# Performance work log

Hardware: AMD Instinct MI355X
Metric: run time of the kernel (lower is better)

## Reference

```python
import jax, jax.numpy as jnp
import numpy as np

B, L, D, W = 4, 512, 768, 12
K = L * W  # number of candidate spans


def _mlp(x, w1, b1, w2, b2):
    # Linear -> ReLU -> (Dropout=identity in eval) -> Linear
    return jax.nn.relu(x @ w1.T + b1) @ w2.T + b2


def setup_inputs() -> dict:
    key = jax.random.key(0)
    ks = jax.random.split(key, 16)
    sc_d = 1.0 / np.sqrt(D)
    sc_4d = 1.0 / np.sqrt(4 * D)
    sc_2d = 1.0 / np.sqrt(2 * D)
    inp = {
        "h": jax.random.normal(ks[0], (B, L, D), dtype=jnp.float32),
        "span_idx": jax.random.randint(ks[1], (B, K, 2), 0, L, dtype=jnp.int64),
        # project_start: Linear(D,4D), Linear(4D,D)
        "ws1": jax.random.uniform(ks[2], (4 * D, D), jnp.float32, -sc_d, sc_d),
        "bs1": jax.random.uniform(ks[3], (4 * D,), jnp.float32, -sc_d, sc_d),
        "ws2": jax.random.uniform(ks[4], (D, 4 * D), jnp.float32, -sc_4d, sc_4d),
        "bs2": jax.random.uniform(ks[5], (D,), jnp.float32, -sc_4d, sc_4d),
        # project_end
        "we1": jax.random.uniform(ks[6], (4 * D, D), jnp.float32, -sc_d, sc_d),
        "be1": jax.random.uniform(ks[7], (4 * D,), jnp.float32, -sc_d, sc_d),
        "we2": jax.random.uniform(ks[8], (D, 4 * D), jnp.float32, -sc_4d, sc_4d),
        "be2": jax.random.uniform(ks[9], (D,), jnp.float32, -sc_4d, sc_4d),
        # out_project: Linear(2D,4D), Linear(4D,D)
        "wo1": jax.random.uniform(ks[10], (4 * D, 2 * D), jnp.float32, -sc_2d, sc_2d),
        "bo1": jax.random.uniform(ks[11], (4 * D,), jnp.float32, -sc_2d, sc_2d),
        "wo2": jax.random.uniform(ks[12], (D, 4 * D), jnp.float32, -sc_4d, sc_4d),
        "bo2": jax.random.uniform(ks[13], (D,), jnp.float32, -sc_4d, sc_4d),
    }
    return inp


def reference(h, span_idx, ws1, bs1, ws2, bs2, we1, be1, we2, be2, wo1, bo1, wo2, bo2):
    start_rep = _mlp(h, ws1, bs1, ws2, bs2)  # [B, L, D]
    end_rep = _mlp(h, we1, be1, we2, be2)    # [B, L, D]
    bidx = jnp.arange(B)[:, None]
    start_span = start_rep[bidx, span_idx[:, :, 0]]  # gather along seq dim -> [B, K, D]
    end_span = end_rep[bidx, span_idx[:, :, 1]]      # [B, K, D]
    cat = jax.nn.relu(jnp.concatenate([start_span, end_span], axis=-1))  # [B, K, 2D]
    out = _mlp(cat, wo1, bo1, wo2, bo2)  # [B, K, D]
    return out.reshape(B, L, W, D)
```

## Files before the change

kernel.cpp:

```cpp
#include <hip/hip_runtime.h>
#include <hip/hip_bf16.h>

using bf16 = __hip_bfloat16;
using bf16x8 = __attribute__((ext_vector_type(8))) __bf16;
using f32x4  = __attribute__((ext_vector_type(4))) float;
using u32x4  = __attribute__((ext_vector_type(4))) unsigned;
typedef unsigned short ushort_t;

#define BM 128
#define BN 128
#define BK 32


__device__ __forceinline__ void gl_lds16(const void* g, void* l) {
  __builtin_amdgcn_global_load_lds(
      (const __attribute__((address_space(1))) void*)g,
      (__attribute__((address_space(3))) void*)l, 16, 0, 0);
}

__device__ __forceinline__ ushort_t f2bf(float f) {
  unsigned u = __float_as_uint(f);
  u += 0x7FFF + ((u >> 16) & 1);
  return (ushort_t)(u >> 16);
}

__global__ void sniff(const unsigned* __restrict__ w1,
                      const unsigned* __restrict__ idx, int* flags) {
  __shared__ int cnt[2];
  if (threadIdx.x == 0) { cnt[0] = 0; cnt[1] = 0; }
  __syncthreads();
  int t = threadIdx.x;
  int c0 = 0;
  for (int k = 0; k < 4; ++k) {
    unsigned lo = w1[t * 4 + k] & 0xFFFFu;
    unsigned e = (lo >> 7) & 0xFF;
    if (e <= 122) c0++;
  }
  int c1 = (idx[2 * t + 1] != 0) ? 1 : 0;
  atomicAdd(&cnt[0], c0);
  atomicAdd(&cnt[1], c1);
  __syncthreads();
  if (threadIdx.x == 0) {
    flags[0] = (cnt[0] >= 900) ? 1 : 0;
    flags[1] = (cnt[1] == 0) ? 1 : 0;
  }
}

__global__ void norm_idx(const int* __restrict__ flags, const void* __restrict__ src,
                         int* __restrict__ dst) {
  int i = blockIdx.x * 256 + threadIdx.x;
  int v = flags[1] ? (int)((const long long*)src)[i] : ((const int*)src)[i];
  dst[i] = v;
}

__global__ void cvt_all(const int* __restrict__ flags,
                        const void* s0, const void* s1, const void* s2,
                        const void* s3, const void* s4, const void* s5,
                        const void* s6, ushort_t* __restrict__ dst) {
  long i = ((long)blockIdx.x * 256 + threadIdx.x) * 4;
  const void* src; long off;
  if      (i <  1572864) { src = s0; off = i; }
  else if (i <  3932160) { src = s1; off = i - 1572864; }
  else if (i <  6291456) { src = s2; off = i - 3932160; }
  else if (i <  8650752) { src = s3; off = i - 6291456; }
  else if (i < 11010048) { src = s4; off = i - 8650752; }
  else if (i < 15728640) { src = s5; off = i - 11010048; }
  else                   { src = s6; off = i - 15728640; }
  if (flags[0]) {
    *(ushort4*)(dst + i) = *((const ushort4*)((const ushort_t*)src + off));
  } else {
    float4 f = ((const float4*)src)[off >> 2];
    ushort4 o;
    o.x = f2bf(f.x); o.y = f2bf(f.y); o.z = f2bf(f.z); o.w = f2bf(f.w);
    *(ushort4*)(dst + i) = o;
  }
}

__global__ void cvt_bias(const int* __restrict__ flags,
                         const void* b0, const void* b1, const void* b2,
                         const void* b3, const void* b4, const void* b5,
                         float* __restrict__ dst) {
  int i = blockIdx.x * 256 + threadIdx.x;
  if (i >= 14592) return;
  if (i >= 11520) { dst[i] = 0.f; return; }
  const void* src; int off;
  if (i < 3072)       { src = b0; off = i; }
  else if (i < 3840)  { src = b1; off = i - 3072; }
  else if (i < 6912)  { src = b2; off = i - 3840; }
  else if (i < 7680)  { src = b3; off = i - 6912; }
  else if (i < 10752) { src = b4; off = i - 7680; }
  else                { src = b5; off = i - 10752; }
  dst[i] = flags[0] ? __bfloat162float(((const bf16*)src)[off])
                    : ((const float*)src)[off];
}

template <bool GATHER, bool RELU, bool OUTF32>
__global__ __launch_bounds__(256) void gemm_bt(
    const bf16* __restrict__ A, const bf16* __restrict__ A2,
    const bf16* __restrict__ repS, const bf16* __restrict__ repE,
    const int* __restrict__ sidx, int row_base,
    const bf16* __restrict__ Bw, const bf16* __restrict__ Bw2,
    const float* __restrict__ bias, const float* __restrict__ bias2,
    void* __restrict__ C, void* __restrict__ C2, int nsplit,
    int N, int Kdim, int bstride) {
  __shared__ bf16 lA[BM * BK];
  __shared__ bf16 lB[BN * BK];

  const int tid  = threadIdx.x;
  const int lane = tid & 63;
  const int wave = tid >> 6;
  const int wm = wave >> 1, wn = wave & 1;
  int by = blockIdx.y;
  const bf16* Bw_ = Bw; const float* bias_ = bias; void* C_ = C; const bf16* A_ = A;
  if (by >= nsplit) { by -= nsplit; Bw_ = Bw2; bias_ = bias2; C_ = C2; A_ = A2; }
  const int m0 = blockIdx.x * BM;
  const int n0 = by * BN;

  const int srow = tid >> 2;
  const int scol = 8 * ((tid & 3) ^ ((tid >> 3) & 3));

  const bf16 *a0 = nullptr, *a1 = nullptr;
  const bf16 *pS0 = nullptr, *pE0 = nullptr, *pS1 = nullptr, *pE1 = nullptr;
  if (GATHER) {
    int r0 = row_base + m0 + srow;
    int r1 = r0 + 64;
    int b0 = r0 / 6144, b1 = r1 / 6144;
    int s0 = min(max(sidx[2 * r0], 0), 511);
    int e0 = min(max(sidx[2 * r0 + 1], 0), 511);
    int s1 = min(max(sidx[2 * r1], 0), 511);
    int e1 = min(max(sidx[2 * r1 + 1], 0), 511);
    pS0 = repS + ((size_t)b0 * 512 + s0) * 768 + scol;
    pE0 = repE + ((size_t)b0 * 512 + e0) * 768 + scol;
    pS1 = repS + ((size_t)b1 * 512 + s1) * 768 + scol;
    pE1 = repE + ((size_t)b1 * 512 + e1) * 768 + scol;
  } else {
    a0 = A_ + (size_t)(m0 + srow) * Kdim + scol;
    a1 = a0 + (size_t)64 * Kdim;
  }
  const bf16* b0p = Bw_ + (size_t)(n0 + srow) * bstride + scol;
  const bf16* b1p = b0p + (size_t)64 * bstride;

  f32x4 acc[4][4];
  const f32x4 z = {0.f, 0.f, 0.f, 0.f};
#pragma unroll
  for (int i = 0; i < 4; ++i)
#pragma unroll
    for (int j = 0; j < 4; ++j) acc[i][j] = z;

  const int fr = lane & 15;
  const int fk = 8 * ((lane >> 4) ^ ((lane >> 1) & 3));

  for (int k0 = 0; k0 < Kdim; k0 += BK) {
    const bf16 *sa0, *sa1;
    if (GATHER) {
      if (k0 < 768) { sa0 = pS0 + k0; sa1 = pS1 + k0; }
      else          { sa0 = pE0 + (k0 - 768); sa1 = pE1 + (k0 - 768); }
    } else {
      sa0 = a0 + k0; sa1 = a1 + k0;
    }
    gl_lds16(sa0, lA + tid * 8);
    gl_lds16(sa1, lA + 2048 + tid * 8);
    gl_lds16(b0p + k0, lB + tid * 8);
    gl_lds16(b1p + k0, lB + 2048 + tid * 8);
    __syncthreads();

    bf16x8 af[4], bv[4];
#pragma unroll
    for (int i = 0; i < 4; ++i)
      af[i] = *(const bf16x8*)(const void*)(lA + (wm * 64 + i * 16 + fr) * BK + fk);
#pragma unroll
    for (int j = 0; j < 4; ++j)
      bv[j] = *(const bf16x8*)(const void*)(lB + (wn * 64 + j * 16 + fr) * BK + fk);
#pragma unroll
    for (int i = 0; i < 4; ++i)
#pragma unroll
      for (int j = 0; j < 4; ++j)
        acc[i][j] = __builtin_amdgcn_mfma_f32_16x16x32_bf16(af[i], bv[j], acc[i][j], 0, 0, 0);
    __syncthreads();
  }

  float* Cf = (float*)C_;
  bf16*  Cb = (bf16*)C_;
#pragma unroll
  for (int j = 0; j < 4; ++j) {
    int n = n0 + wn * 64 + j * 16 + fr;
    float bj = bias_[n];
#pragma unroll
    for (int i = 0; i < 4; ++i) {
      int mb = m0 + wm * 64 + i * 16 + (lane >> 4) * 4;
#pragma unroll
      for (int r = 0; r < 4; ++r) {
        float v = acc[i][j][r] + bj;
        if (RELU) v = fmaxf(v, 0.f);
        if (OUTF32) Cf[(size_t)(mb + r) * N + n] = v;
        else        Cb[(size_t)(mb + r) * N + n] = __float2bfloat16(v);
      }
    }
  }
}

__global__ __launch_bounds__(256) void gemm_bt64(
    const bf16* __restrict__ A, const bf16* __restrict__ A2,
    const bf16* __restrict__ Bw, const bf16* __restrict__ Bw2,
    const float* __restrict__ bias, const float* __restrict__ bias2,
    bf16* __restrict__ C, bf16* __restrict__ C2, int nsplit,
    int N, int Kdim) {
  __shared__ bf16 lA[64 * BK];
  __shared__ bf16 lB[64 * BK];

  const int tid  = threadIdx.x;
  const int lane = tid & 63;
  const int wave = tid >> 6;
  const int wm = wave >> 1, wn = wave & 1;
  int by = blockIdx.y;
  const bf16* Bw_ = Bw; const float* bias_ = bias; bf16* C_ = C; const bf16* A_ = A;
  if (by >= nsplit) { by -= nsplit; Bw_ = Bw2; bias_ = bias2; C_ = C2; A_ = A2; }
  const int m0 = blockIdx.x * 64;
  const int n0 = by * 64;

  const int srow = tid >> 2;
  const int scol = 8 * ((tid & 3) ^ ((tid >> 3) & 3));

  const bf16* ap = A_  + (size_t)(m0 + srow) * Kdim + scol;
  const bf16* bp = Bw_ + (size_t)(n0 + srow) * Kdim + scol;

  f32x4 acc[2][2];
  const f32x4 z = {0.f, 0.f, 0.f, 0.f};
#pragma unroll
  for (int i = 0; i < 2; ++i)
#pragma unroll
    for (int j = 0; j < 2; ++j) acc[i][j] = z;

  const int fr = lane & 15;
  const int fk = 8 * ((lane >> 4) ^ ((lane >> 1) & 3));

  for (int k0 = 0; k0 < Kdim; k0 += BK) {
    gl_lds16(ap + k0, lA + tid * 8);
    gl_lds16(bp + k0, lB + tid * 8);
    __syncthreads();

    bf16x8 af[2], bv[2];
#pragma unroll
    for (int i = 0; i < 2; ++i)
      af[i] = *(const bf16x8*)(const void*)(lA + (wm * 32 + i * 16 + fr) * BK + fk);
#pragma unroll
    for (int j = 0; j < 2; ++j)
      bv[j] = *(const bf16x8*)(const void*)(lB + (wn * 32 + j * 16 + fr) * BK + fk);
#pragma unroll
    for (int i = 0; i < 2; ++i)
#pragma unroll
      for (int j = 0; j < 2; ++j)
        acc[i][j] = __builtin_amdgcn_mfma_f32_16x16x32_bf16(af[i], bv[j], acc[i][j], 0, 0, 0);
    __syncthreads();
  }

#pragma unroll
  for (int j = 0; j < 2; ++j) {
    int n = n0 + wn * 32 + j * 16 + fr;
    float bj = bias_[n];
#pragma unroll
    for (int i = 0; i < 2; ++i) {
      int mb = m0 + wm * 32 + i * 16 + (lane >> 4) * 4;
#pragma unroll
      for (int r = 0; r < 4; ++r) {
        float v = fmaxf(acc[i][j][r] + bj, 0.f);
        C_[(size_t)(mb + r) * N + n] = __float2bfloat16(v);
      }
    }
  }
}

__global__ __launch_bounds__(512) void gemm_final_fused(
    const ushort_t* __restrict__ Ps, const ushort_t* __restrict__ Pe,
    const int* __restrict__ sidx,
    const bf16* __restrict__ Bw, const float* __restrict__ bias,
    float* __restrict__ out) {
  __shared__ bf16 lA[2 * 4096];
  __shared__ bf16 lB[2 * 16384];

  const int tid  = threadIdx.x;
  const int lane = tid & 63;
  const int wave = tid >> 6;
  const int wm = wave >> 2, wn = wave & 3;
  const int m0 = blockIdx.x * 64;
  const int n0 = blockIdx.y * 256;

  const int t8   = tid & 255;
  const int ksub = tid >> 8;
  const int srow = t8 >> 2;
  const int scol = 8 * ((t8 & 3) ^ ((t8 >> 3) & 3));

  int r0 = m0 + srow;
  int b0 = r0 / 6144;
  int s0 = min(max(sidx[2 * r0], 0), 511);
  int e0 = min(max(sidx[2 * r0 + 1], 0), 511);
  const ushort_t* pS0 = Ps + ((size_t)b0 * 512 + s0) * 3072 + ksub * 32 + scol;
  const ushort_t* pE0 = Pe + ((size_t)b0 * 512 + e0) * 3072 + ksub * 32 + scol;
  const int aoff = ksub * 2048 + t8 * 8;

  const bf16* bp = Bw + (size_t)(n0 + srow) * 3072 + ksub * 32 + scol;
  const int boff = ksub * 8192 + t8 * 8;

  f32x4 acc[2][4];
  const f32x4 z = {0.f, 0.f, 0.f, 0.f};
#pragma unroll
  for (int i = 0; i < 2; ++i)
#pragma unroll
    for (int j = 0; j < 4; ++j) acc[i][j] = z;

  const int fr = lane & 15;
  const int fk = 8 * ((lane >> 4) ^ ((lane >> 1) & 3));

  auto pack_store = [&](u32x4 xs, u32x4 xe, bf16* dst) {
    u32x4 wv;
#pragma unroll
    for (int q = 0; q < 4; ++q) {
      float lo = fmaxf(__uint_as_float(xs[q] << 16) + __uint_as_float(xe[q] << 16), 0.f);
      float hi = fmaxf(__uint_as_float(xs[q] & 0xFFFF0000u) +
                       __uint_as_float(xe[q] & 0xFFFF0000u), 0.f);
      unsigned w;
      asm("v_cvt_pk_bf16_f32 %0, %1, %2" : "=v"(w) : "v"(lo), "v"(hi));
      wv[q] = w;
    }
    *(u32x4*)(void*)dst = wv;
  };

  auto stageB = [&](int k0, int buf) {
#pragma unroll
    for (int g = 0; g < 4; ++g)
      gl_lds16(bp + (size_t)g * 64 * 3072 + k0, lB + buf + boff + g * 2048);
  };

  {
    u32x4 xs = *(const u32x4*)(const void*)pS0;
    u32x4 xe = *(const u32x4*)(const void*)pE0;
    stageB(0, 0);
    pack_store(xs, xe, lA + aoff);
    __syncthreads();
  }

  for (int it = 0; it < 48; ++it) {
    const int curA = (it & 1) << 12;
    const int curB = (it & 1) << 14;
    const int nxtA = curA ^ 4096;
    const int nxtB = curB ^ 16384;
    const int k1 = (it + 1) * 64;
    const bool pre = (it + 1) < 48;
    u32x4 xs, xe;
    if (pre) {
      xs = *(const u32x4*)(const void*)(pS0 + k1);
      xe = *(const u32x4*)(const void*)(pE0 + k1);
      stageB(k1, nxtB);
    }

#pragma unroll
    for (int s = 0; s < 2; ++s) {
      bf16x8 af[2];
#pragma unroll
      for (int i = 0; i < 2; ++i)
        af[i] = *(const bf16x8*)(const void*)(
            lA + curA + s * 2048 + (wm * 32 + i * 16 + fr) * 32 + fk);
#pragma unroll
      for (int j = 0; j < 4; ++j) {
        bf16x8 bv = *(const bf16x8*)(const void*)(
            lB + curB + s * 8192 + (wn * 64 + j * 16 + fr) * 32 + fk);
#pragma unroll
        for (int i = 0; i < 2; ++i)
          acc[i][j] = __builtin_amdgcn_mfma_f32_16x16x32_bf16(af[i], bv, acc[i][j], 0, 0, 0);
      }
    }

    if (pre) {
      pack_store(xs, xe, lA + nxtA + aoff);
    }
    __syncthreads();
  }

#pragma unroll
  for (int j = 0; j < 4; ++j) {
    int n = n0 + wn * 64 + j * 16 + fr;
    float bj = bias[n];
#pragma unroll
    for (int i = 0; i < 2; ++i) {
      int mb = m0 + wm * 32 + i * 16 + (lane >> 4) * 4;
#pragma unroll
      for (int r = 0; r < 4; ++r)
        out[(size_t)(mb + r) * 768 + n] = acc[i][j][r] + bj;
    }
  }
}

extern "C" void kernel_launch(void* const* d_in, const int* in_sizes, int n_in,
                              void* d_out, int out_size, void* d_ws, size_t ws_size,
                              hipStream_t stream) {
  const void* h    = d_in[0];
  const void* sidx = d_in[1];
  const void *ws1 = d_in[2],  *bs1 = d_in[3];
  const void *ws2 = d_in[4],  *bs2 = d_in[5];
  const void *we1 = d_in[6],  *be1 = d_in[7];
  const void *we2 = d_in[8],  *be2 = d_in[9];
  const void *wo1 = d_in[10], *bo1 = d_in[11];
  const void *wo2 = d_in[12], *bo2 = d_in[13];

  char* p = (char*)d_ws;
  int*      flags = (int*)p;
  int*      idx32 = (int*)(p + 256);
  float*    biasf = (float*)(p + 256 + 196608);
  ushort_t* hb    = (ushort_t*)(p + 256 + 196608 + 65536);
  ushort_t* w1sb  = hb   + (size_t)1572864;
  ushort_t* w2sb  = w1sb + (size_t)2359296;
  ushort_t* w1eb  = w2sb + (size_t)2359296;
  ushort_t* w2eb  = w1eb + (size_t)2359296;
  ushort_t* wo1b  = w2eb + (size_t)2359296;
  ushort_t* wo2b  = wo1b + (size_t)4718592;
  ushort_t* repS  = wo2b + (size_t)2359296;
  ushort_t* repE  = repS + (size_t)1572864;
  char*     R     = (char*)(repE + (size_t)1572864);
  size_t fixed = (size_t)(R - (char*)d_ws);
  if (ws_size < fixed) return;
  size_t Rsz = ws_size - fixed;

  const size_t P_BF = (size_t)2 * 2048 * 3072 * 2;
  int tier = (Rsz >= P_BF) ? 2 : 3;

  dim3 blk(256);
  const int XBIG = 0x40000000;
  sniff<<<1, blk, 0, stream>>>((const unsigned*)ws1, (const unsigned*)sidx, flags);
  norm_idx<<<192, blk, 0, stream>>>(flags, sidx, idx32);
  cvt_all<<<17664, blk, 0, stream>>>(flags, h, ws1, ws2, we1, we2, wo1, wo2, hb);
  cvt_bias<<<57, blk, 0, stream>>>(flags, bs1, bs2, be1, be2, bo1, bo2, biasf);
  const float *bs1f = biasf, *bs2f = biasf + 3072, *be1f = biasf + 3840,
              *be2f = biasf + 6912, *bo1f = biasf + 7680, *bo2f = biasf + 10752,
              *zerof = biasf + 11520;
  float* outf = (float*)d_out;

  if (tier == 2) {
    ushort_t* hidS = (ushort_t*)R;
    ushort_t* hidE = hidS + (size_t)2048 * 3072;
    gemm_bt<false, true, false><<<dim3(16, 48), blk, 0, stream>>>(
        (const bf16*)hb, (const bf16*)hb, nullptr, nullptr, nullptr, 0,
        (const bf16*)w1sb, (const bf16*)w1eb, bs1f, be1f,
        hidS, hidE, 24, 3072, 768, 768);
    gemm_bt64<<<dim3(32, 24), blk, 0, stream>>>(
        (const bf16*)hidS, (const bf16*)hidE,
        (const bf16*)w2sb, (const bf16*)w2eb, bs2f, be2f,
        (bf16*)repS, (bf16*)repE, 12, 768, 3072);
    ushort_t* Ps = (ushort_t*)R;
    ushort_t* Pe = Ps + (size_t)2048 * 3072;
    gemm_bt<false, false, false><<<dim3(16, 48), blk, 0, stream>>>(
        (const bf16*)repS, (const bf16*)repE, nullptr, nullptr, nullptr, 0,
        (const bf16*)wo1b, (const bf16*)wo1b + 768, bo1f, zerof,
        Ps, Pe, 24, 3072, 768, 1536);
    gemm_final_fused<<<dim3(384, 3), dim3(512), 0, stream>>>(
        Ps, Pe, idx32, (const bf16*)wo2b, bo2f, outf);
  } else {
    long long cT = (long long)(Rsz / ((size_t)2 * 3072 * 2));
    cT = (cT / 128) * 128; if (cT > 2048) cT = 2048;
    long long cO = (long long)(Rsz / ((size_t)3072 * 2));
    cO = (cO / 128) * 128; if (cO > 24576) cO = 24576;
    if (cT < 128 || cO < 128) return;
    ushort_t* scr = (ushort_t*)R;
    for (long long r = 0; r < 2048; r += cT) {
      long long mc = 2048 - r < cT ? 2048 - r : cT;
      ushort_t* hidS = scr;
      ushort_t* hidE = scr + (size_t)cT * 3072;
      gemm_bt<false, true, false><<<dim3(mc / 128, 48), blk, 0, stream>>>(
          (const bf16*)hb + r * 768, (const bf16*)hb + r * 768,
          nullptr, nullptr, nullptr, 0,
          (const bf16*)w1sb, (const bf16*)w1eb, bs1f, be1f,
          hidS, hidE, 24, 3072, 768, 768);
      gemm_bt<false, true, false><<<dim3(mc / 128, 12), blk, 0, stream>>>(
          (const bf16*)hidS, (const bf16*)hidE, nullptr, nullptr, nullptr, 0,
          (const bf16*)w2sb, (const bf16*)w2eb, bs2f, be2f,
          (bf16*)repS + r * 768, (bf16*)repE + r * 768, 6, 768, 3072, 3072);
    }
    for (long long r = 0; r < 24576; r += cO) {
      long long mc = 24576 - r < cO ? 24576 - r : cO;
      gemm_bt<true, true, false><<<dim3(mc / 128, 24), blk, 0, stream>>>(
          nullptr, nullptr, (const bf16*)repS, (const bf16*)repE, idx32, (int)r,
          (const bf16*)wo1b, nullptr, bo1f, nullptr,
          scr, nullptr, XBIG, 3072, 1536, 1536);
      gemm_bt<false, false, true><<<dim3(mc / 128, 6), blk, 0, stream>>>(
          (const bf16*)scr, nullptr, nullptr, nullptr, nullptr, 0,
          (const bf16*)wo2b, nullptr, bo2f, nullptr,
          outf + (size_t)r * 768, nullptr, XBIG, 768, 3072, 3072);
    }
  }
}
```

Measured before the change: 474.2 us.

## Enlarge final fused GEMM tile to 128x256 with single-stage BK=32 k-loop

Each block of the final fused gather-GEMM now covers 128 rows instead of 64, so each wave holds a 4x4 MFMA accumulator tile. The k-step shrinks from 64 to 32, giving 96 iterations. This halves the number of blocks and the B-weight traffic per output row, and raises MFMA work per LDS load. The cost is more accumulator registers, lower occupancy, and twice as many barrier-separated iterations.

```diff
diff --git a/kernel.cpp b/kernel.cpp
--- a/kernel.cpp
+++ b/kernel.cpp
@@ -276,35 +276,32 @@
     const bf16* __restrict__ Bw, const float* __restrict__ bias,
     float* __restrict__ out) {
   __shared__ bf16 lA[2 * 4096];
-  __shared__ bf16 lB[2 * 16384];
+  __shared__ bf16 lB[2 * 8192];
 
   const int tid  = threadIdx.x;
   const int lane = tid & 63;
   const int wave = tid >> 6;
   const int wm = wave >> 2, wn = wave & 3;
-  const int m0 = blockIdx.x * 64;
+  const int m0 = blockIdx.x * 128;
   const int n0 = blockIdx.y * 256;
 
-  const int t8   = tid & 255;
-  const int ksub = tid >> 8;
-  const int srow = t8 >> 2;
-  const int scol = 8 * ((t8 & 3) ^ ((t8 >> 3) & 3));
+  const int srow = tid >> 2;
+  const int scol = 8 * ((tid & 3) ^ ((tid >> 3) & 3));
 
   int r0 = m0 + srow;
   int b0 = r0 / 6144;
   int s0 = min(max(sidx[2 * r0], 0), 511);
   int e0 = min(max(sidx[2 * r0 + 1], 0), 511);
-  const ushort_t* pS0 = Ps + ((size_t)b0 * 512 + s0) * 3072 + ksub * 32 + scol;
-  const ushort_t* pE0 = Pe + ((size_t)b0 * 512 + e0) * 3072 + ksub * 32 + scol;
-  const int aoff = ksub * 2048 + t8 * 8;
-
-  const bf16* bp = Bw + (size_t)(n0 + srow) * 3072 + ksub * 32 + scol;
-  const int boff = ksub * 8192 + t8 * 8;
-
-  f32x4 acc[2][4];
+  const ushort_t* pS0 = Ps + ((size_t)b0 * 512 + s0) * 3072 + scol;
+  const ushort_t* pE0 = Pe + ((size_t)b0 * 512 + e0) * 3072 + scol;
+
+  const bf16* bp0 = Bw + (size_t)(n0 + srow) * 3072 + scol;
+  const bf16* bp1 = bp0 + (size_t)128 * 3072;
+
+  f32x4 acc[4][4];
   const f32x4 z = {0.f, 0.f, 0.f, 0.f};
 #pragma unroll
-  for (int i = 0; i < 2; ++i)
+  for (int i = 0; i < 4; ++i)
 #pragma unroll
     for (int j = 0; j < 4; ++j) acc[i][j] = z;
 
@@ -325,53 +322,47 @@
     *(u32x4*)(void*)dst = wv;
   };
 
-  auto stageB = [&](int k0, int buf) {
-#pragma unroll
-    for (int g = 0; g < 4; ++g)
-      gl_lds16(bp + (size_t)g * 64 * 3072 + k0, lB + buf + boff + g * 2048);
-  };
-
   {
     u32x4 xs = *(const u32x4*)(const void*)pS0;
     u32x4 xe = *(const u32x4*)(const void*)pE0;
-    stageB(0, 0);
-    pack_store(xs, xe, lA + aoff);
-    __syncthreads();
-  }
-
-  for (int it = 0; it < 48; ++it) {
+    gl_lds16(bp0, lB + tid * 8);
+    gl_lds16(bp1, lB + 4096 + tid * 8);
+    pack_store(xs, xe, lA + tid * 8);
+    __syncthreads();
+  }
+
+  for (int it = 0; it < 96; ++it) {
     const int curA = (it & 1) << 12;
-    const int curB = (it & 1) << 14;
+    const int curB = (it & 1) << 13;
     const int nxtA = curA ^ 4096;
-    const int nxtB = curB ^ 16384;
-    const int k1 = (it + 1) * 64;
-    const bool pre = (it + 1) < 48;
+    const int nxtB = curB ^ 8192;
+    const int k1 = (it + 1) * BK;
+    const bool pre = (it + 1) < 96;
     u32x4 xs, xe;
     if (pre) {
       xs = *(const u32x4*)(const void*)(pS0 + k1);
       xe = *(const u32x4*)(const void*)(pE0 + k1);
-      stageB(k1, nxtB);
-    }
-
-#pragma unroll
-    for (int s = 0; s < 2; ++s) {
-      bf16x8 af[2];
-#pragma unroll
-      for (int i = 0; i < 2; ++i)
-        af[i] = *(const bf16x8*)(const void*)(
-            lA + curA + s * 2048 + (wm * 32 + i * 16 + fr) * 32 + fk);
-#pragma unroll
-      for (int j = 0; j < 4; ++j) {
-        bf16x8 bv = *(const bf16x8*)(const void*)(
-            lB + curB + s * 8192 + (wn * 64 + j * 16 + fr) * 32 + fk);
-#pragma unroll
-        for (int i = 0; i < 2; ++i)
-          acc[i][j] = __builtin_amdgcn_mfma_f32_16x16x32_bf16(af[i], bv, acc[i][j], 0, 0, 0);
-      }
-    }
+      gl_lds16(bp0 + k1, lB + nxtB + tid * 8);
+      gl_lds16(bp1 + k1, lB + nxtB + 4096 + tid * 8);
+    }
+
+    bf16x8 af[4], bv[4];
+#pragma unroll
+    for (int i = 0; i < 4; ++i)
+      af[i] = *(const bf16x8*)(const void*)(
+          lA + curA + (wm * 64 + i * 16 + fr) * BK + fk);
+#pragma unroll
+    for (int j = 0; j < 4; ++j)
+      bv[j] = *(const bf16x8*)(const void*)(
+          lB + curB + (wn * 64 + j * 16 + fr) * BK + fk);
+#pragma unroll
+    for (int i = 0; i < 4; ++i)
+#pragma unroll
+      for (int j = 0; j < 4; ++j)
+        acc[i][j] = __builtin_amdgcn_mfma_f32_16x16x32_bf16(af[i], bv[j], acc[i][j], 0, 0, 0);
 
     if (pre) {
-      pack_store(xs, xe, lA + nxtA + aoff);
+      pack_store(xs, xe, lA + nxtA + tid * 8);
     }
     __syncthreads();
   }
@@ -381,8 +372,8 @@
     int n = n0 + wn * 64 + j * 16 + fr;
     float bj = bias[n];
 #pragma unroll
-    for (int i = 0; i < 2; ++i) {
-      int mb = m0 + wm * 32 + i * 16 + (lane >> 4) * 4;
+    for (int i = 0; i < 4; ++i) {
+      int mb = m0 + wm * 64 + i * 16 + (lane >> 4) * 4;
 #pragma unroll
       for (int r = 0; r < 4; ++r)
         out[(size_t)(mb + r) * 768 + n] = acc[i][j][r] + bj;
@@ -451,7 +442,7 @@
         (const bf16*)repS, (const bf16*)repE, nullptr, nullptr, nullptr, 0,
         (const bf16*)wo1b, (const bf16*)wo1b + 768, bo1f, zerof,
         Ps, Pe, 24, 3072, 768, 1536);
-    gemm_final_fused<<<dim3(384, 3), dim3(512), 0, stream>>>(
+    gemm_final_fused<<<dim3(192, 3), dim3(512), 0, stream>>>(
         Ps, Pe, idx32, (const bf16*)wo2b, bo2f, outf);
   } else {
     long long cT = (long long)(Rsz / ((size_t)2 * 3072 * 2));
```

Measured after the change: 470.6 us. Within noise of the previous version (-0.8%).
